# Kernel optimization log

Hardware: AMD Instinct MI355X
Metric: run time of the kernel (lower is better)

## Reference

```python
import jax, jax.numpy as jnp
import numpy as np

V = 50257   # vocab_size
D = 768     # d_model
NL = 4      # n_layers
DI = 1536   # d_inner = expand * d_model
DS = 16     # d_state
DC = 4      # d_conv
B = 2       # batch
L = 512     # seq_len
EPS = 1e-5  # RMSNorm eps
STD = 0.02  # init std


def setup_inputs() -> dict:
    key = jax.random.key(0)
    ks = jax.random.split(key, 8)
    idx = jax.random.randint(ks[0], (B, L), 0, V)
    emb = jax.random.normal(ks[1], (V, D), dtype=jnp.float32) * STD          # tied embedding / lm_head
    W_in = jax.random.normal(ks[2], (NL, 2 * DI, D), dtype=jnp.float32) * STD
    conv_w = jax.random.normal(ks[3], (NL, DI, 1, DC), dtype=jnp.float32) * STD  # depthwise conv [O,I/g,K]
    W_xproj = jax.random.normal(ks[4], (NL, 2 * DS + 1, DI), dtype=jnp.float32) * STD
    W_dt = jax.random.normal(ks[5], (NL, DI, 1), dtype=jnp.float32) * STD    # dt_rank = 1
    b_dt = jnp.zeros((NL, DI), dtype=jnp.float32)
    a_log = jnp.tile(jnp.log(jnp.arange(1, DS + 1, dtype=jnp.float32)), (NL, DI, 1))
    d_param = jnp.ones((NL, DI), dtype=jnp.float32)
    W_out = jax.random.normal(ks[6], (NL, D, DI), dtype=jnp.float32) * STD
    norm_w = jnp.ones((D,), dtype=jnp.float32)
    return dict(idx=idx, emb=emb, W_in=W_in, conv_w=conv_w, W_xproj=W_xproj,
                W_dt=W_dt, b_dt=b_dt, a_log=a_log, d_param=d_param,
                W_out=W_out, norm_w=norm_w)


def _mamba_block(x, W_in, conv_w, W_xproj, W_dt, b_dt, a_log, d_param, W_out):
    # in_proj + split into x, z
    xz = jnp.einsum('bld,ed->ble', x, W_in)            # [B,L,2*DI]
    xs, z = jnp.split(xz, 2, axis=-1)
    # causal depthwise conv1d (torch pads d_conv-1 both sides, keeps first L -> left pad only)
    xc = jnp.transpose(xs, (0, 2, 1))                  # [B,DI,L]
    xc = jax.lax.conv_general_dilated(xc, conv_w, window_strides=(1,),
                                      padding=[(DC - 1, 0)],
                                      feature_group_count=DI,
                                      dimension_numbers=('NCH', 'OIH', 'NCH'))
    xs = jax.nn.silu(jnp.transpose(xc, (0, 2, 1)))     # [B,L,DI]
    # selective SSM
    A = -jnp.exp(a_log)                                # [DI,DS]
    xp = jnp.einsum('bld,ed->ble', xs, W_xproj)        # [B,L,2*DS+1]
    dt_raw = xp[..., 0]                                # [B,L]
    Bp = xp[..., 1:1 + DS]                             # [B,L,DS]
    Cp = xp[..., 1 + DS:]                              # [B,L,DS]
    delta = jax.nn.softplus(dt_raw[..., None] * W_dt[:, 0] + b_dt)  # [B,L,DI]

    def step(h, inp):
        d_i, b_i, c_i, x_i = inp                       # [B,DI],[B,DS],[B,DS],[B,DI]
        a_bar = jnp.exp(d_i[:, :, None] * A)           # [B,DI,DS]
        h = a_bar * h + d_i[:, :, None] * b_i[:, None, :] * x_i[:, :, None]
        y = jnp.einsum('bn,bdn->bd', c_i, h) + d_param * x_i
        return h, y

    h0 = jnp.zeros((x.shape[0], DI, DS), dtype=x.dtype)
    seq = (jnp.moveaxis(delta, 1, 0), jnp.moveaxis(Bp, 1, 0),
           jnp.moveaxis(Cp, 1, 0), jnp.moveaxis(xs, 1, 0))
    _, ys = jax.lax.scan(step, h0, seq)
    y = jnp.moveaxis(ys, 0, 1)                         # [B,L,DI]
    y = y * jax.nn.silu(z)
    return jnp.einsum('ble,de->bld', y, W_out)         # [B,L,D]


def reference(idx, emb, W_in, conv_w, W_xproj, W_dt, b_dt, a_log, d_param, W_out, norm_w):
    x = emb[idx]                                       # [B,L,D]

    def layer(carry, p):
        w_in, c_w, w_xp, w_dt, bdt, alog, dpar, w_out = p
        out = carry + _mamba_block(carry, w_in, c_w, w_xp, w_dt, bdt, alog, dpar, w_out)
        return out, None

    x, _ = jax.lax.scan(layer, x, (W_in, conv_w, W_xproj, W_dt, b_dt, a_log, d_param, W_out))
    rms = jax.lax.rsqrt(jnp.mean(x * x, axis=-1, keepdims=True) + EPS)
    x = x * rms * norm_w
    logits = jnp.einsum('bld,vd->blv', x, emb)         # tied lm_head
    return logits
```

## Files before the change

### kernel.cpp

```cpp
#include <hip/hip_runtime.h>
#include <cstdint>

#define VV     50257
#define VPAD   50432
#define DMODEL 768
#define NLAYER 4
#define DINNER 1536
#define DSTATE 16
#define DCONV  4
#define BATCH  2
#define SEQ    512
#define MROWS  (BATCH*SEQ)
#define XZS    ((long)MROWS * 2 * DINNER)

typedef unsigned short u16;
typedef __attribute__((ext_vector_type(8))) short bf16x8;
typedef __attribute__((ext_vector_type(4))) float f32x4;

__device__ __forceinline__ u16 f2bf(float f) {
  unsigned u = __float_as_uint(f);
  u += 0x7fffu + ((u >> 16) & 1u);
  return (u16)(u >> 16);
}

__device__ __forceinline__ void async16(const void* g, void* l) {
  auto gp = reinterpret_cast<const __attribute__((address_space(1))) unsigned int*>(
      reinterpret_cast<uintptr_t>(g));
  auto lp = reinterpret_cast<__attribute__((address_space(3))) unsigned int*>(
      reinterpret_cast<uintptr_t>(l));
  __builtin_amdgcn_global_load_lds(gp, lp, 16, 0, 0);
}

__global__ void prep_kern(const float* __restrict__ emb, const float* __restrict__ W_in,
                          const float* __restrict__ W_out, const int* __restrict__ idx,
                          u16* __restrict__ embbf, u16* __restrict__ winbf,
                          u16* __restrict__ woutbf, float* __restrict__ xf,
                          u16* __restrict__ xbf) {
  const int E4  = VPAD * DMODEL / 4;
  const int W14 = NLAYER * 2 * DINNER * DMODEL / 4;
  const int W24 = NLAYER * DMODEL * DINNER / 4;
  const int X4  = MROWS * DMODEL / 4;
  const int TOT = E4 + W14 + W24 + X4;
  int i = blockIdx.x * blockDim.x + threadIdx.x;
  const int stride = gridDim.x * blockDim.x;
  for (; i < TOT; i += stride) {
    if (i < E4) {
      ushort4 o;
      if (i < VV * DMODEL / 4) {
        float4 v = *(const float4*)(emb + (long)i * 4);
        o.x = f2bf(v.x); o.y = f2bf(v.y); o.z = f2bf(v.z); o.w = f2bf(v.w);
      } else { o.x = 0; o.y = 0; o.z = 0; o.w = 0; }
      *(ushort4*)(embbf + (long)i * 4) = o;
    } else if (i < E4 + W14) {
      const int j = i - E4;
      float4 v = *(const float4*)(W_in + (long)j * 4);
      ushort4 o; o.x = f2bf(v.x); o.y = f2bf(v.y); o.z = f2bf(v.z); o.w = f2bf(v.w);
      *(ushort4*)(winbf + (long)j * 4) = o;
    } else if (i < E4 + W14 + W24) {
      const int j = i - E4 - W14;
      float4 v = *(const float4*)(W_out + (long)j * 4);
      ushort4 o; o.x = f2bf(v.x); o.y = f2bf(v.y); o.z = f2bf(v.z); o.w = f2bf(v.w);
      *(ushort4*)(woutbf + (long)j * 4) = o;
    } else {
      const int j = i - E4 - W14 - W24;
      const int r = j / (DMODEL / 4);
      const int c = (j % (DMODEL / 4)) * 4;
      const int id = idx[r];
      float4 v = *(const float4*)(emb + (long)id * DMODEL + c);
      *(float4*)(xf + (long)r * DMODEL + c) = v;
      ushort4 o; o.x = f2bf(v.x); o.y = f2bf(v.y); o.z = f2bf(v.z); o.w = f2bf(v.w);
      *(ushort4*)(xbf + (long)r * DMODEL + c) = o;
    }
  }
}

template<bool GUARDN, bool XSWZ>
__global__ __launch_bounds__(256) void gemm3_kern(
    const u16* __restrict__ A, const u16* __restrict__ B,
    float* __restrict__ C, int M, int N, int K, int lda, int ldb)
{
  __shared__ u16 As[3][128 * 32];
  __shared__ u16 Bs[3][128 * 32];
  int bx, by;
  if (XSWZ) {
    const int nt = gridDim.x >> 3;
    const int t = (blockIdx.x & 7) * nt + (blockIdx.x >> 3);
    bx = t & 7; by = t >> 3;
  } else { bx = blockIdx.x; by = blockIdx.y; }
  const int koff = blockIdx.z * K;
  const long coff = (long)blockIdx.z * M * N;

  const int tid  = threadIdx.x;
  const int wave = tid >> 6;
  const int lane = tid & 63;
  const int wr = wave >> 1, wc = wave & 1;
  const int m0 = bx * 128;
  const int n0 = by * 128;

  const int srow = wave * 32 + (lane >> 2);
  const int sblk = ((lane & 3) ^ ((lane >> 3) & 3)) * 8;

  f32x4 acc[4][4];
#pragma unroll
  for (int i = 0; i < 4; ++i)
#pragma unroll
    for (int j = 0; j < 4; ++j) acc[i][j] = (f32x4){0.f, 0.f, 0.f, 0.f};

  const int arow = wr * 64 + (lane & 15);
  const int brow = wc * 64 + (lane & 15);
  const int sa   = (((lane >> 4) ^ ((lane >> 1) & 3)) << 3);

  const int KT = K / 32;
  auto stage = [&](int kt) {
    const int slot = kt % 3;
    const long kcol = (long)koff + kt * 32;
#pragma unroll
    for (int j = 0; j < 2; ++j) {
      async16(A + (long)(m0 + srow + j * 16) * lda + kcol + sblk,
              (char*)(As[slot]) + (wave * 32 + j * 16) * 64);
      async16(B + (long)(n0 + srow + j * 16) * ldb + kcol + sblk,
              (char*)(Bs[slot]) + (wave * 32 + j * 16) * 64);
    }
  };

  stage(0);
  stage(1);
  for (int t = 0; t < KT; ++t) {
    if (t + 2 < KT) {
      stage(t + 2);
      asm volatile("s_waitcnt vmcnt(8)" ::: "memory");
    } else if (t + 2 == KT) {
      asm volatile("s_waitcnt vmcnt(4)" ::: "memory");
    } else {
      asm volatile("s_waitcnt vmcnt(0)" ::: "memory");
    }
    __builtin_amdgcn_s_barrier();
    asm volatile("" ::: "memory");

    const u16* as = As[t % 3];
    const u16* bs = Bs[t % 3];
    bf16x8 af[4], bv[4];
#pragma unroll
    for (int i = 0; i < 4; ++i) af[i] = *(const bf16x8*)(as + (arow + 16 * i) * 32 + sa);
#pragma unroll
    for (int j = 0; j < 4; ++j) bv[j] = *(const bf16x8*)(bs + (brow + 16 * j) * 32 + sa);

    __builtin_amdgcn_s_setprio(1);
#pragma unroll
    for (int i = 0; i < 4; ++i)
#pragma unroll
      for (int j = 0; j < 4; ++j)
        acc[i][j] = __builtin_amdgcn_mfma_f32_16x16x32_bf16(af[i], bv[j], acc[i][j], 0, 0, 0);
    __builtin_amdgcn_s_setprio(0);

    asm volatile("" ::: "memory");
    __builtin_amdgcn_s_barrier();
    asm volatile("" ::: "memory");
  }

  const int rbase = m0 + wr * 64 + ((lane >> 4) << 2);
  const int cbase = n0 + wc * 64 + (lane & 15);
#pragma unroll
  for (int j = 0; j < 4; ++j) {
    const int col = cbase + j * 16;
    if (GUARDN && col >= N) continue;
#pragma unroll
    for (int i = 0; i < 4; ++i) {
#pragma unroll
      for (int r = 0; r < 4; ++r) {
        const int row = rbase + i * 16 + r;
        C[coff + (long)row * N + col] = acc[i][j][r];
      }
    }
  }
}

__global__ __launch_bounds__(512, 2) void gemm8_kern(
    const u16* __restrict__ A, const u16* __restrict__ B,
    float* __restrict__ C, int N, int K, int lda, int ldb)
{
  __shared__ u16 lds[2][2][256 * 64];
  const int tid = threadIdx.x;
  const int wave = tid >> 6;
  const int lane = tid & 63;
  const int wm = wave >> 2, wn = wave & 3;

  const int nwg = gridDim.x;
  const int q = nwg >> 3, r = nwg & 7;
  const int xcd = blockIdx.x & 7;
  const int t = (xcd < r ? xcd * (q + 1) : r * (q + 1) + (xcd - r) * q) + (blockIdx.x >> 3);
  const int m0 = (t & 3) * 256;
  const int n0 = (t >> 2) * 256;

  const int NT = K / 64;

  const int sblk = (((lane & 7) ^ (lane >> 3)) << 3);
  auto stage = [&](int buf, int ab, int half, int kt) {
    const u16* Mat = ab ? B : A;
    const int ld = ab ? ldb : lda;
    const int tb = ab ? n0 : m0;
#pragma unroll
    for (int j = 0; j < 2; ++j) {
      const int rloc = half * 128 + j * 64 + wave * 8;
      async16(Mat + (long)(tb + rloc + (lane >> 3)) * ld + kt * 64 + sblk,
              (char*)&lds[buf][ab][0] + (rloc << 7));
    }
  };

  bf16x8 af[4][2], bl[2][2], bh[2][2];
  const int aq = lane >> 4;
  auto readA = [&](int buf, int half) {
#pragma unroll
    for (int mf = 0; mf < 4; ++mf) {
      const int rr = half * 128 + wm * 64 + mf * 16 + (lane & 15);
#pragma unroll
      for (int ks = 0; ks < 2; ++ks) {
        const int q2 = ks * 4 + aq;
        af[mf][ks] = *(const bf16x8*)(&lds[buf][0][0] + rr * 64 + ((q2 ^ (rr & 7)) << 3));
      }
    }
  };
  auto readB = [&](int buf, int half, bf16x8 (&bf)[2][2]) {
#pragma unroll
    for (int nf = 0; nf < 2; ++nf) {
      const int rr = half * 128 + wn * 32 + nf * 16 + (lane & 15);
#pragma unroll
      for (int ks = 0; ks < 2; ++ks) {
        const int q2 = ks * 4 + aq;
        bf[nf][ks] = *(const bf16x8*)(&lds[buf][1][0] + rr * 64 + ((q2 ^ (rr & 7)) << 3));
      }
    }
  };

  f32x4 acc[8][4];
#pragma unroll
  for (int i = 0; i < 8; ++i)
#pragma unroll
    for (int j = 0; j < 4; ++j) acc[i][j] = (f32x4){0.f, 0.f, 0.f, 0.f};

#define MFMA16(QM, QN, BF)                                                        \
  __builtin_amdgcn_s_setprio(1);                                                  \
  _Pragma("unroll")                                                               \
  for (int mf = 0; mf < 4; ++mf)                                                  \
    _Pragma("unroll")                                                             \
    for (int nf = 0; nf < 2; ++nf)                                                \
      _Pragma("unroll")                                                           \
      for (int ks = 0; ks < 2; ++ks)                                              \
        acc[(QM)*4+mf][(QN)*2+nf] = __builtin_amdgcn_mfma_f32_16x16x32_bf16(      \
            af[mf][ks], BF[nf][ks], acc[(QM)*4+mf][(QN)*2+nf], 0, 0, 0);          \
  __builtin_amdgcn_s_setprio(0);

#define BAR()   asm volatile("" ::: "memory"); __builtin_amdgcn_s_barrier(); asm volatile("" ::: "memory")
#define WAITV(NN) asm volatile("s_waitcnt vmcnt(" #NN ")" ::: "memory"); __builtin_amdgcn_sched_barrier(0)
#define WAITL(NN) asm volatile("s_waitcnt lgkmcnt(" #NN ")" ::: "memory"); __builtin_amdgcn_sched_barrier(0)

  stage(0, 0, 0, 0); stage(0, 1, 0, 0); stage(0, 1, 1, 0); stage(0, 0, 1, 0);
  stage(1, 0, 0, 1); stage(1, 1, 0, 1); stage(1, 1, 1, 1);
  WAITV(6);
  BAR();
  readB(0, 0, bl);

#define TILE(KTE, BUF)                                                            \
  {                                                                               \
    const int kt = (KTE);                                                         \
    if (kt >= NT - 2) { WAITV(0); } else { WAITV(8); }                            \
    BAR();                                                                        \
    readA(BUF, 0);                                                                \
    readB(BUF, 1, bh);                                                            \
    if (kt + 1 < NT) stage(BUF ^ 1, 0, 1, kt + 1);                                \
    WAITL(4);                                                                     \
    MFMA16(0, 0, bl);                                                             \
    BAR();                                                                        \
    if (kt + 2 < NT) stage(BUF, 0, 0, kt + 2);                                    \
    WAITL(0);                                                                     \
    MFMA16(0, 1, bh);                                                             \
    if (kt >= NT - 2) { WAITV(0); } else { WAITV(10); }                           \
    BAR();                                                                        \
    readA(BUF, 1);                                                                \
    if (kt + 2 < NT) stage(BUF, 1, 0, kt + 2);                                    \
    WAITL(0);                                                                     \
    MFMA16(1, 0, bl);                                                             \
    if (kt >= NT - 2) { WAITV(0); } else { WAITV(8); }                            \
    BAR();                                                                        \
    if (kt + 1 < NT) readB(BUF ^ 1, 0, bl);                                       \
    if (kt + 2 < NT) stage(BUF, 1, 1, kt + 2);                                    \
    WAITL(4);                                                                     \
    MFMA16(1, 1, bh);                                                             \
  }

  for (int kt2 = 0; kt2 < NT; kt2 += 2) {
    TILE(kt2, 0);
    TILE(kt2 + 1, 1);
  }

#pragma unroll
  for (int qm = 0; qm < 2; ++qm)
#pragma unroll
    for (int mf = 0; mf < 4; ++mf)
#pragma unroll
      for (int qn = 0; qn < 2; ++qn)
#pragma unroll
        for (int nf = 0; nf < 2; ++nf) {
          const int col = n0 + qn * 128 + wn * 32 + nf * 16 + (lane & 15);
          if (col >= N) continue;
          const int row0 = m0 + qm * 128 + wm * 64 + mf * 16 + ((lane >> 4) << 2);
          const f32x4 v = acc[qm * 4 + mf][qn * 2 + nf];
#pragma unroll
          for (int rr2 = 0; rr2 < 4; ++rr2)
            C[(long)(row0 + rr2) * N + col] = v[rr2];
        }
#undef TILE
#undef MFMA16
#undef BAR
#undef WAITV
#undef WAITL
}

__global__ __launch_bounds__(256) void redout_kern(const float* __restrict__ part,
                                                   float* __restrict__ xf,
                                                   u16* __restrict__ xbf) {
  const int i = blockIdx.x * blockDim.x + threadIdx.x;
  if (i >= MROWS * DMODEL / 4) return;
  const int stride4 = MROWS * DMODEL / 4;
  float4 s = ((const float4*)part)[i];
  float4 p1 = ((const float4*)part)[i + stride4];
  float4 p2 = ((const float4*)part)[i + 2 * stride4];
  float4 p3 = ((const float4*)part)[i + 3 * stride4];
  float4 x = ((const float4*)xf)[i];
  s.x += p1.x + p2.x + p3.x + x.x;
  s.y += p1.y + p2.y + p3.y + x.y;
  s.z += p1.z + p2.z + p3.z + x.z;
  s.w += p1.w + p2.w + p3.w + x.w;
  ((float4*)xf)[i] = s;
  ushort4 o; o.x = f2bf(s.x); o.y = f2bf(s.y); o.z = f2bf(s.z); o.w = f2bf(s.w);
  ((ushort4*)xbf)[i] = o;
}

__global__ __launch_bounds__(256) void convxproj_kern(
    const float* __restrict__ xz, const float* __restrict__ cw,
    const float* __restrict__ Wx, const float* __restrict__ wdt,
    const float* __restrict__ bdt,
    float* __restrict__ xs, float* __restrict__ dlt, float* __restrict__ bc)
{
  __shared__ float sx[DINNER];
  __shared__ float sxp[40];
  const int row = blockIdx.x;
  const int t = row & (SEQ - 1);
  const int tid = threadIdx.x;

  for (int c = tid; c < DINNER; c += 256) {
    const float* w = cw + c * DCONV;
    float a = 0.f;
#pragma unroll
    for (int k = 0; k < DCONV; ++k) {
      const int tt = t - (DCONV - 1) + k;
      if (tt >= 0) {
        const long ix = (long)(row - (DCONV - 1) + k) * (2 * DINNER) + c;
        a += w[k] * (xz[ix] + xz[ix + XZS]);
      }
    }
    const float s = a / (1.f + __expf(-a));
    sx[c] = s;
    xs[(long)row * DINNER + c] = s;
  }
  __syncthreads();

  const int wv = tid >> 6, lane = tid & 63;
  for (int e = wv; e < 2 * DSTATE + 1; e += 4) {
    const float* We = Wx + (long)e * DINNER;
    float p = 0.f;
    for (int d = lane; d < DINNER; d += 64) p += sx[d] * We[d];
#pragma unroll
    for (int off = 32; off; off >>= 1) p += __shfl_xor(p, off, 64);
    if (lane == 0) sxp[e] = p;
  }
  __syncthreads();
  const float dtr = sxp[0];
  for (int d = tid; d < DINNER; d += 256) {
    float v = dtr * wdt[d] + bdt[d];
    float sp = (v > 15.f) ? v : log1pf(__expf(v));
    dlt[(long)row * DINNER + d] = sp;
  }
  if (tid < 2 * DSTATE) bc[(long)row * (2 * DSTATE) + tid] = sxp[1 + tid];
}

__global__ __launch_bounds__(256) void scan_kern(
    const float* __restrict__ dlt, const float* __restrict__ bc,
    const float* __restrict__ xs, const float* __restrict__ xz,
    const float* __restrict__ alog, const float* __restrict__ dpar,
    u16* __restrict__ ybf)
{
  __shared__ float sh_h[32][8][DSTATE];
  __shared__ float sh_s[32][8];
  const int tid = threadIdx.x;
  const int ch = tid & 7, chunk = tid >> 3;
  const int ch_abs = blockIdx.x * 8 + ch;
  const int b = ch_abs / DINNER, d = ch_abs % DINNER;
  float An[DSTATE];
#pragma unroll
  for (int n = 0; n < DSTATE; ++n) An[n] = -__expf(alog[(long)d * DSTATE + n]);
  const int r0 = b * SEQ + chunk * 16;

  float h[DSTATE];
#pragma unroll
  for (int n = 0; n < DSTATE; ++n) h[n] = 0.f;
  float ssum = 0.f;
  for (int s = 0; s < 16; ++s) {
    const int row = r0 + s;
    const float dl = dlt[(long)row * DINNER + d];
    const float xv = xs[(long)row * DINNER + d];
    const float dx = dl * xv;
    const float4* bp = (const float4*)(bc + (long)row * (2 * DSTATE));
    float Bv[DSTATE];
    *(float4*)&Bv[0] = bp[0]; *(float4*)&Bv[4] = bp[1];
    *(float4*)&Bv[8] = bp[2]; *(float4*)&Bv[12] = bp[3];
    ssum += dl;
#pragma unroll
    for (int n = 0; n < DSTATE; ++n) h[n] = __expf(dl * An[n]) * h[n] + dx * Bv[n];
  }
#pragma unroll
  for (int n = 0; n < DSTATE; ++n) sh_h[chunk][ch][n] = h[n];
  sh_s[chunk][ch] = ssum;
  __syncthreads();

  if (tid < 128) {
    const int n2 = tid & 15, ch2 = tid >> 4;
    const int d2 = (blockIdx.x * 8 + ch2) % DINNER;
    const float A2 = -__expf(alog[(long)d2 * DSTATE + n2]);
    float carry = 0.f;
    for (int c = 0; c < 32; ++c) {
      const float hl = sh_h[c][ch2][n2];
      sh_h[c][ch2][n2] = carry;
      carry = __expf(A2 * sh_s[c][ch2]) * carry + hl;
    }
  }
  __syncthreads();

#pragma unroll
  for (int n = 0; n < DSTATE; ++n) h[n] = sh_h[chunk][ch][n];
  const float dp = dpar[d];
  for (int s = 0; s < 16; ++s) {
    const int row = r0 + s;
    const float dl = dlt[(long)row * DINNER + d];
    const float xv = xs[(long)row * DINNER + d];
    const float dx = dl * xv;
    const float4* bp = (const float4*)(bc + (long)row * (2 * DSTATE));
    float Bv[DSTATE], Cv[DSTATE];
    *(float4*)&Bv[0] = bp[0]; *(float4*)&Bv[4] = bp[1];
    *(float4*)&Bv[8] = bp[2]; *(float4*)&Bv[12] = bp[3];
    *(float4*)&Cv[0] = bp[4]; *(float4*)&Cv[4] = bp[5];
    *(float4*)&Cv[8] = bp[6]; *(float4*)&Cv[12] = bp[7];
    float y = 0.f;
#pragma unroll
    for (int n = 0; n < DSTATE; ++n) {
      const float hn = __expf(dl * An[n]) * h[n] + dx * Bv[n];
      h[n] = hn;
      y += Cv[n] * hn;
    }
    y += dp * xv;
    const long zix = (long)row * (2 * DINNER) + DINNER + d;
    const float zz = xz[zix] + xz[zix + XZS];
    const float o = y * (zz / (1.f + __expf(-zz)));
    ybf[(long)row * DINNER + d] = f2bf(o);
  }
}

__global__ __launch_bounds__(256) void rmsfuse_kern(const float* __restrict__ part,
                                                    const float* __restrict__ xf,
                                                    const float* __restrict__ nw,
                                                    u16* __restrict__ xnbf) {
  const int row = blockIdx.x, tid = threadIdx.x;
  const int S = MROWS * DMODEL;
  float v[3];
  float p = 0.f;
#pragma unroll
  for (int k = 0; k < 3; ++k) {
    const int i = row * DMODEL + tid + k * 256;
    float x = xf[i] + part[i] + part[i + S] + part[i + 2 * S] + part[i + 3 * S];
    v[k] = x;
    p += x * x;
  }
#pragma unroll
  for (int off = 32; off; off >>= 1) p += __shfl_xor(p, off, 64);
  __shared__ float red[4];
  __shared__ float s_rms;
  const int wv = tid >> 6, lane = tid & 63;
  if (lane == 0) red[wv] = p;
  __syncthreads();
  if (tid == 0) {
    float tsum = red[0] + red[1] + red[2] + red[3];
    s_rms = rsqrtf(tsum / (float)DMODEL + 1e-5f);
  }
  __syncthreads();
  const float r = s_rms;
#pragma unroll
  for (int k = 0; k < 3; ++k) {
    const int dd = tid + k * 256;
    xnbf[(long)row * DMODEL + dd] = f2bf(v[k] * r * nw[dd]);
  }
}

extern "C" void kernel_launch(void* const* d_in, const int* in_sizes, int n_in,
                              void* d_out, int out_size, void* d_ws, size_t ws_size,
                              hipStream_t stream)
{
  (void)in_sizes; (void)n_in; (void)out_size; (void)ws_size;
  const int*   idx   = (const int*)  d_in[0];
  const float* emb   = (const float*)d_in[1];
  const float* W_in  = (const float*)d_in[2];
  const float* convw = (const float*)d_in[3];
  const float* W_xp  = (const float*)d_in[4];
  const float* W_dt  = (const float*)d_in[5];
  const float* b_dt  = (const float*)d_in[6];
  const float* a_log = (const float*)d_in[7];
  const float* d_par = (const float*)d_in[8];
  const float* W_out = (const float*)d_in[9];
  const float* normw = (const float*)d_in[10];
  float* out = (float*)d_out;

  char* ws = (char*)d_ws;
  size_t off = 0;
  auto alloc = [&](size_t bytes) -> void* {
    void* p = ws + off;
    off += (bytes + 255) & ~(size_t)255;
    return p;
  };
  u16*   embbf  = (u16*)  alloc((size_t)VPAD * DMODEL * 2);
  u16*   winbf  = (u16*)  alloc((size_t)NLAYER * 2 * DINNER * DMODEL * 2);
  u16*   woutbf = (u16*)  alloc((size_t)NLAYER * DMODEL * DINNER * 2);
  float* xf     = (float*)alloc((size_t)MROWS * DMODEL * 4);
  u16*   xbf    = (u16*)  alloc((size_t)MROWS * DMODEL * 2);
  float* xz     = (float*)alloc((size_t)2 * MROWS * 2 * DINNER * 4);
  float* xs     = (float*)alloc((size_t)MROWS * DINNER * 4);
  float* dlt    = (float*)alloc((size_t)MROWS * DINNER * 4);
  float* bc     = (float*)alloc((size_t)MROWS * 2 * DSTATE * 4);
  u16*   ybf    = (u16*)  alloc((size_t)MROWS * DINNER * 2);
  u16*   xnbf   = (u16*)  alloc((size_t)MROWS * DMODEL * 2);
  float* part   = (float*)alloc((size_t)4 * MROWS * DMODEL * 4);

  prep_kern<<<2048, 256, 0, stream>>>(emb, W_in, W_out, idx, embbf, winbf, woutbf, xf, xbf);

  for (int l = 0; l < NLAYER; ++l) {
    gemm3_kern<false, true><<<dim3(8 * (2 * DINNER / 128), 1, 2), 256, 0, stream>>>(
        xbf, winbf + (size_t)l * 2 * DINNER * DMODEL, xz,
        MROWS, 2 * DINNER, DMODEL / 2, DMODEL, DMODEL);
    convxproj_kern<<<MROWS, 256, 0, stream>>>(
        xz, convw + (size_t)l * DINNER * DCONV,
        W_xp + (size_t)l * (2 * DSTATE + 1) * DINNER,
        W_dt + (size_t)l * DINNER, b_dt + (size_t)l * DINNER, xs, dlt, bc);
    scan_kern<<<BATCH * DINNER / 8, 256, 0, stream>>>(
        dlt, bc, xs, xz, a_log + (size_t)l * DINNER * DSTATE, d_par + (size_t)l * DINNER, ybf);
    gemm3_kern<false, true><<<dim3(8 * (DMODEL / 128), 1, 4), 256, 0, stream>>>(
        ybf, woutbf + (size_t)l * DMODEL * DINNER, part,
        MROWS, DMODEL, DINNER / 4, DINNER, DINNER);
    if (l < NLAYER - 1)
      redout_kern<<<MROWS * DMODEL / 4 / 256, 256, 0, stream>>>(part, xf, xbf);
  }
  rmsfuse_kern<<<MROWS, 256, 0, stream>>>(part, xf, normw, xnbf);
  gemm8_kern<<<4 * (VPAD / 256), 512, 0, stream>>>(
      xnbf, embbf, out, VV, DMODEL, DMODEL, DMODEL);
}
```

Measured before the change: 794.5 us.

## Fuse residual add into out-proj via atomics and read fp32 activations in in-proj

Result: slower. 816.2 us (+2.7%).

```diff
diff --git a/kernel.cpp b/kernel.cpp
--- a/kernel.cpp
+++ b/kernel.cpp
@@ -34,8 +34,7 @@
 __global__ void prep_kern(const float* __restrict__ emb, const float* __restrict__ W_in,
                           const float* __restrict__ W_out, const int* __restrict__ idx,
                           u16* __restrict__ embbf, u16* __restrict__ winbf,
-                          u16* __restrict__ woutbf, float* __restrict__ xf,
-                          u16* __restrict__ xbf) {
+                          u16* __restrict__ woutbf, float* __restrict__ xf) {
   const int E4  = VPAD * DMODEL / 4;
   const int W14 = NLAYER * 2 * DINNER * DMODEL / 4;
   const int W24 = NLAYER * DMODEL * DINNER / 4;
@@ -68,27 +67,135 @@
       const int id = idx[r];
       float4 v = *(const float4*)(emb + (long)id * DMODEL + c);
       *(float4*)(xf + (long)r * DMODEL + c) = v;
-      ushort4 o; o.x = f2bf(v.x); o.y = f2bf(v.y); o.z = f2bf(v.z); o.w = f2bf(v.w);
-      *(ushort4*)(xbf + (long)r * DMODEL + c) = o;
-    }
-  }
-}
-
-template<bool GUARDN, bool XSWZ>
+    }
+  }
+}
+
+__global__ __launch_bounds__(256) void gemmf_kern(
+    const float* __restrict__ A, const u16* __restrict__ B,
+    float* __restrict__ C, int M, int N, int K, int lda, int ldb)
+{
+  __shared__ float Af[3][128 * 32];
+  __shared__ u16   Bs[3][128 * 32];
+  const int nt = gridDim.x >> 3;
+  const int t = (blockIdx.x & 7) * nt + (blockIdx.x >> 3);
+  const int bx = t & 7, by = t >> 3;
+  const int koff = blockIdx.z * K;
+  const long coff = (long)blockIdx.z * M * N;
+
+  const int tid  = threadIdx.x;
+  const int wave = tid >> 6;
+  const int lane = tid & 63;
+  const int wr = wave >> 1, wc = wave & 1;
+  const int m0 = bx * 128;
+  const int n0 = by * 128;
+
+  const int sblkA = (((lane & 7) ^ (lane >> 3)) << 2);
+  const int srowB = wave * 32 + (lane >> 2);
+  const int sblkB = ((lane & 3) ^ ((lane >> 3) & 3)) * 8;
+
+  f32x4 acc[4][4];
+#pragma unroll
+  for (int i = 0; i < 4; ++i)
+#pragma unroll
+    for (int j = 0; j < 4; ++j) acc[i][j] = (f32x4){0.f, 0.f, 0.f, 0.f};
+
+  const int arow = wr * 64 + (lane & 15);
+  const int brow = wc * 64 + (lane & 15);
+  const int saB  = (((lane >> 4) ^ ((lane >> 1) & 3)) << 3);
+  const int g2   = (lane >> 4) << 1;
+
+  const int KT = K / 32;
+  auto stage = [&](int kt) {
+    const int slot = kt % 3;
+    const long kcol = (long)koff + kt * 32;
+#pragma unroll
+    for (int j = 0; j < 4; ++j) {
+      const int rloc = wave * 32 + j * 8;
+      async16(A + (long)(m0 + rloc + (lane >> 3)) * lda + kcol + sblkA,
+              (char*)(Af[slot]) + rloc * 128);
+    }
+#pragma unroll
+    for (int j = 0; j < 2; ++j) {
+      async16(B + (long)(n0 + srowB + j * 16) * ldb + kcol + sblkB,
+              (char*)(Bs[slot]) + (wave * 32 + j * 16) * 64);
+    }
+  };
+
+  stage(0);
+  stage(1);
+  for (int t2 = 0; t2 < KT; ++t2) {
+    if (t2 + 2 < KT) {
+      stage(t2 + 2);
+      asm volatile("s_waitcnt vmcnt(12)" ::: "memory");
+    } else if (t2 + 2 == KT) {
+      asm volatile("s_waitcnt vmcnt(6)" ::: "memory");
+    } else {
+      asm volatile("s_waitcnt vmcnt(0)" ::: "memory");
+    }
+    __builtin_amdgcn_s_barrier();
+    asm volatile("" ::: "memory");
+
+    const float* af_l = Af[t2 % 3];
+    const u16*   bs_l = Bs[t2 % 3];
+    bf16x8 av[4], bv[4];
+#pragma unroll
+    for (int i = 0; i < 4; ++i) {
+      const int rr = arow + 16 * i;
+      const float* rp = af_l + rr * 32;
+      const f32x4 lo = *(const f32x4*)(rp + ((g2 ^ (rr & 7)) << 2));
+      const f32x4 hi = *(const f32x4*)(rp + (((g2 + 1) ^ (rr & 7)) << 2));
+      bf16x8 a;
+      a[0] = (short)f2bf(lo[0]); a[1] = (short)f2bf(lo[1]);
+      a[2] = (short)f2bf(lo[2]); a[3] = (short)f2bf(lo[3]);
+      a[4] = (short)f2bf(hi[0]); a[5] = (short)f2bf(hi[1]);
+      a[6] = (short)f2bf(hi[2]); a[7] = (short)f2bf(hi[3]);
+      av[i] = a;
+    }
+#pragma unroll
+    for (int j = 0; j < 4; ++j) bv[j] = *(const bf16x8*)(bs_l + (brow + 16 * j) * 32 + saB);
+
+    __builtin_amdgcn_s_setprio(1);
+#pragma unroll
+    for (int i = 0; i < 4; ++i)
+#pragma unroll
+      for (int j = 0; j < 4; ++j)
+        acc[i][j] = __builtin_amdgcn_mfma_f32_16x16x32_bf16(av[i], bv[j], acc[i][j], 0, 0, 0);
+    __builtin_amdgcn_s_setprio(0);
+
+    asm volatile("" ::: "memory");
+    __builtin_amdgcn_s_barrier();
+    asm volatile("" ::: "memory");
+  }
+
+  const int rbase = m0 + wr * 64 + ((lane >> 4) << 2);
+  const int cbase = n0 + wc * 64 + (lane & 15);
+#pragma unroll
+  for (int j = 0; j < 4; ++j) {
+    const int col = cbase + j * 16;
+#pragma unroll
+    for (int i = 0; i < 4; ++i) {
+#pragma unroll
+      for (int r = 0; r < 4; ++r) {
+        const int row = rbase + i * 16 + r;
+        C[coff + (long)row * N + col] = acc[i][j][r];
+      }
+    }
+  }
+}
+
+template<bool ATOMIC>
 __global__ __launch_bounds__(256) void gemm3_kern(
     const u16* __restrict__ A, const u16* __restrict__ B,
     float* __restrict__ C, int M, int N, int K, int lda, int ldb)
 {
   __shared__ u16 As[3][128 * 32];
   __shared__ u16 Bs[3][128 * 32];
-  int bx, by;
-  if (XSWZ) {
-    const int nt = gridDim.x >> 3;
-    const int t = (blockIdx.x & 7) * nt + (blockIdx.x >> 3);
-    bx = t & 7; by = t >> 3;
-  } else { bx = blockIdx.x; by = blockIdx.y; }
+  const int nt = gridDim.x >> 3;
+  const int t = (blockIdx.x & 7) * nt + (blockIdx.x >> 3);
+  const int bx = t & 7, by = t >> 3;
   const int koff = blockIdx.z * K;
-  const long coff = (long)blockIdx.z * M * N;
+  const long coff = ATOMIC ? 0 : (long)blockIdx.z * M * N;
 
   const int tid  = threadIdx.x;
   const int wave = tid >> 6;
@@ -125,11 +232,11 @@
 
   stage(0);
   stage(1);
-  for (int t = 0; t < KT; ++t) {
-    if (t + 2 < KT) {
-      stage(t + 2);
+  for (int t2 = 0; t2 < KT; ++t2) {
+    if (t2 + 2 < KT) {
+      stage(t2 + 2);
       asm volatile("s_waitcnt vmcnt(8)" ::: "memory");
-    } else if (t + 2 == KT) {
+    } else if (t2 + 2 == KT) {
       asm volatile("s_waitcnt vmcnt(4)" ::: "memory");
     } else {
       asm volatile("s_waitcnt vmcnt(0)" ::: "memory");
@@ -137,8 +244,8 @@
     __builtin_amdgcn_s_barrier();
     asm volatile("" ::: "memory");
 
-    const u16* as = As[t % 3];
-    const u16* bs = Bs[t % 3];
+    const u16* as = As[t2 % 3];
+    const u16* bs = Bs[t2 % 3];
     bf16x8 af[4], bv[4];
 #pragma unroll
     for (int i = 0; i < 4; ++i) af[i] = *(const bf16x8*)(as + (arow + 16 * i) * 32 + sa);
@@ -163,13 +270,18 @@
 #pragma unroll
   for (int j = 0; j < 4; ++j) {
     const int col = cbase + j * 16;
-    if (GUARDN && col >= N) continue;
 #pragma unroll
     for (int i = 0; i < 4; ++i) {
 #pragma unroll
       for (int r = 0; r < 4; ++r) {
         const int row = rbase + i * 16 + r;
-        C[coff + (long)row * N + col] = acc[i][j][r];
+        const long off = coff + (long)row * N + col;
+        if (ATOMIC) {
+          __hip_atomic_fetch_add(&C[off], acc[i][j][r], __ATOMIC_RELAXED,
+                                 __HIP_MEMORY_SCOPE_AGENT);
+        } else {
+          C[off] = acc[i][j][r];
+        }
       }
     }
   }
@@ -316,26 +428,6 @@
 #undef WAITL
 }
 
-__global__ __launch_bounds__(256) void redout_kern(const float* __restrict__ part,
-                                                   float* __restrict__ xf,
-                                                   u16* __restrict__ xbf) {
-  const int i = blockIdx.x * blockDim.x + threadIdx.x;
-  if (i >= MROWS * DMODEL / 4) return;
-  const int stride4 = MROWS * DMODEL / 4;
-  float4 s = ((const float4*)part)[i];
-  float4 p1 = ((const float4*)part)[i + stride4];
-  float4 p2 = ((const float4*)part)[i + 2 * stride4];
-  float4 p3 = ((const float4*)part)[i + 3 * stride4];
-  float4 x = ((const float4*)xf)[i];
-  s.x += p1.x + p2.x + p3.x + x.x;
-  s.y += p1.y + p2.y + p3.y + x.y;
-  s.z += p1.z + p2.z + p3.z + x.z;
-  s.w += p1.w + p2.w + p3.w + x.w;
-  ((float4*)xf)[i] = s;
-  ushort4 o; o.x = f2bf(s.x); o.y = f2bf(s.y); o.z = f2bf(s.z); o.w = f2bf(s.w);
-  ((ushort4*)xbf)[i] = o;
-}
-
 __global__ __launch_bounds__(256) void convxproj_kern(
     const float* __restrict__ xz, const float* __restrict__ cw,
     const float* __restrict__ Wx, const float* __restrict__ wdt,
@@ -465,20 +557,17 @@
   }
 }
 
-__global__ __launch_bounds__(256) void rmsfuse_kern(const float* __restrict__ part,
-                                                    const float* __restrict__ xf,
-                                                    const float* __restrict__ nw,
-                                                    u16* __restrict__ xnbf) {
+__global__ __launch_bounds__(256) void rms_kern(const float* __restrict__ xf,
+                                                const float* __restrict__ nw,
+                                                u16* __restrict__ xnbf) {
   const int row = blockIdx.x, tid = threadIdx.x;
-  const int S = MROWS * DMODEL;
   float v[3];
   float p = 0.f;
 #pragma unroll
   for (int k = 0; k < 3; ++k) {
     const int i = row * DMODEL + tid + k * 256;
-    float x = xf[i] + part[i] + part[i + S] + part[i + 2 * S] + part[i + 3 * S];
-    v[k] = x;
-    p += x * x;
+    v[k] = xf[i];
+    p += v[k] * v[k];
   }
 #pragma unroll
   for (int off = 32; off; off >>= 1) p += __shfl_xor(p, off, 64);
@@ -529,20 +618,18 @@
   u16*   winbf  = (u16*)  alloc((size_t)NLAYER * 2 * DINNER * DMODEL * 2);
   u16*   woutbf = (u16*)  alloc((size_t)NLAYER * DMODEL * DINNER * 2);
   float* xf     = (float*)alloc((size_t)MROWS * DMODEL * 4);
-  u16*   xbf    = (u16*)  alloc((size_t)MROWS * DMODEL * 2);
   float* xz     = (float*)alloc((size_t)2 * MROWS * 2 * DINNER * 4);
   float* xs     = (float*)alloc((size_t)MROWS * DINNER * 4);
   float* dlt    = (float*)alloc((size_t)MROWS * DINNER * 4);
   float* bc     = (float*)alloc((size_t)MROWS * 2 * DSTATE * 4);
   u16*   ybf    = (u16*)  alloc((size_t)MROWS * DINNER * 2);
   u16*   xnbf   = (u16*)  alloc((size_t)MROWS * DMODEL * 2);
-  float* part   = (float*)alloc((size_t)4 * MROWS * DMODEL * 4);
-
-  prep_kern<<<2048, 256, 0, stream>>>(emb, W_in, W_out, idx, embbf, winbf, woutbf, xf, xbf);
+
+  prep_kern<<<2048, 256, 0, stream>>>(emb, W_in, W_out, idx, embbf, winbf, woutbf, xf);
 
   for (int l = 0; l < NLAYER; ++l) {
-    gemm3_kern<false, true><<<dim3(8 * (2 * DINNER / 128), 1, 2), 256, 0, stream>>>(
-        xbf, winbf + (size_t)l * 2 * DINNER * DMODEL, xz,
+    gemmf_kern<<<dim3(8 * (2 * DINNER / 128), 1, 2), 256, 0, stream>>>(
+        xf, winbf + (size_t)l * 2 * DINNER * DMODEL, xz,
         MROWS, 2 * DINNER, DMODEL / 2, DMODEL, DMODEL);
     convxproj_kern<<<MROWS, 256, 0, stream>>>(
         xz, convw + (size_t)l * DINNER * DCONV,
@@ -550,13 +637,11 @@
         W_dt + (size_t)l * DINNER, b_dt + (size_t)l * DINNER, xs, dlt, bc);
     scan_kern<<<BATCH * DINNER / 8, 256, 0, stream>>>(
         dlt, bc, xs, xz, a_log + (size_t)l * DINNER * DSTATE, d_par + (size_t)l * DINNER, ybf);
-    gemm3_kern<false, true><<<dim3(8 * (DMODEL / 128), 1, 4), 256, 0, stream>>>(
-        ybf, woutbf + (size_t)l * DMODEL * DINNER, part,
+    gemm3_kern<true><<<dim3(8 * (DMODEL / 128), 1, 4), 256, 0, stream>>>(
+        ybf, woutbf + (size_t)l * DMODEL * DINNER, xf,
         MROWS, DMODEL, DINNER / 4, DINNER, DINNER);
-    if (l < NLAYER - 1)
-      redout_kern<<<MROWS * DMODEL / 4 / 256, 256, 0, stream>>>(part, xf, xbf);
-  }
-  rmsfuse_kern<<<MROWS, 256, 0, stream>>>(part, xf, normw, xnbf);
+  }
+  rms_kern<<<MROWS, 256, 0, stream>>>(xf, normw, xnbf);
   gemm8_kern<<<4 * (VPAD / 256), 512, 0, stream>>>(
       xnbf, embbf, out, VV, DMODEL, DMODEL, DMODEL);
 }
```

## Replace lm_head GEMM with 256x128 tile, 2-stage pipeline, higher occupancy

Applied to the files above, without the earlier changes.

New measurement: 813.7 us. +2.4%, slower.

```diff
diff --git a/kernel.cpp b/kernel.cpp
--- a/kernel.cpp
+++ b/kernel.cpp
@@ -125,11 +125,11 @@
 
   stage(0);
   stage(1);
-  for (int t = 0; t < KT; ++t) {
-    if (t + 2 < KT) {
-      stage(t + 2);
+  for (int t2 = 0; t2 < KT; ++t2) {
+    if (t2 + 2 < KT) {
+      stage(t2 + 2);
       asm volatile("s_waitcnt vmcnt(8)" ::: "memory");
-    } else if (t + 2 == KT) {
+    } else if (t2 + 2 == KT) {
       asm volatile("s_waitcnt vmcnt(4)" ::: "memory");
     } else {
       asm volatile("s_waitcnt vmcnt(0)" ::: "memory");
@@ -137,8 +137,8 @@
     __builtin_amdgcn_s_barrier();
     asm volatile("" ::: "memory");
 
-    const u16* as = As[t % 3];
-    const u16* bs = Bs[t % 3];
+    const u16* as = As[t2 % 3];
+    const u16* bs = Bs[t2 % 3];
     bf16x8 af[4], bv[4];
 #pragma unroll
     for (int i = 0; i < 4; ++i) af[i] = *(const bf16x8*)(as + (arow + 16 * i) * 32 + sa);
@@ -175,145 +175,106 @@
   }
 }
 
-__global__ __launch_bounds__(512, 2) void gemm8_kern(
+__global__ __launch_bounds__(512, 4) void gemm9_kern(
     const u16* __restrict__ A, const u16* __restrict__ B,
     float* __restrict__ C, int N, int K, int lda, int ldb)
 {
-  __shared__ u16 lds[2][2][256 * 64];
+  __shared__ u16 As[2][256 * 32];
+  __shared__ u16 Bs[2][128 * 32];
   const int tid = threadIdx.x;
   const int wave = tid >> 6;
   const int lane = tid & 63;
-  const int wm = wave >> 2, wn = wave & 3;
-
-  const int nwg = gridDim.x;
-  const int q = nwg >> 3, r = nwg & 7;
-  const int xcd = blockIdx.x & 7;
-  const int t = (xcd < r ? xcd * (q + 1) : r * (q + 1) + (xcd - r) * q) + (blockIdx.x >> 3);
+  const int wm = wave >> 1, wn = wave & 1;
+
+  const int nt = gridDim.x >> 3;
+  const int t = (blockIdx.x & 7) * nt + (blockIdx.x >> 3);
   const int m0 = (t & 3) * 256;
-  const int n0 = (t >> 2) * 256;
-
-  const int NT = K / 64;
-
-  const int sblk = (((lane & 7) ^ (lane >> 3)) << 3);
-  auto stage = [&](int buf, int ab, int half, int kt) {
-    const u16* Mat = ab ? B : A;
-    const int ld = ab ? ldb : lda;
-    const int tb = ab ? n0 : m0;
+  const int n0 = (t >> 2) * 128;
+
+  const int NT = K / 32;
+
+  auto stage = [&](int buf, int kt) {
+    const long kc = (long)kt * 32;
 #pragma unroll
     for (int j = 0; j < 2; ++j) {
-      const int rloc = half * 128 + j * 64 + wave * 8;
-      async16(Mat + (long)(tb + rloc + (lane >> 3)) * ld + kt * 64 + sblk,
-              (char*)&lds[buf][ab][0] + (rloc << 7));
+      const int rl = wave * 32 + j * 16 + (lane >> 2);
+      const int sb = (((lane & 3) ^ ((rl >> 1) & 3)) << 3);
+      async16(A + (long)(m0 + rl) * lda + kc + sb,
+              (char*)(As[buf]) + (wave * 32 + j * 16) * 64);
+    }
+    {
+      const int rl = wave * 16 + (lane >> 2);
+      const int sb = (((lane & 3) ^ ((rl >> 1) & 3)) << 3);
+      async16(B + (long)(n0 + rl) * ldb + kc + sb,
+              (char*)(Bs[buf]) + (wave * 16) * 64);
     }
   };
 
-  bf16x8 af[4][2], bl[2][2], bh[2][2];
+  f32x4 acc[4][4];
+#pragma unroll
+  for (int i = 0; i < 4; ++i)
+#pragma unroll
+    for (int j = 0; j < 4; ++j) acc[i][j] = (f32x4){0.f, 0.f, 0.f, 0.f};
+
   const int aq = lane >> 4;
-  auto readA = [&](int buf, int half) {
+  const int lrow = lane & 15;
+
+  stage(0, 0);
+  stage(1, 1);
+  for (int kt = 0; kt < NT; ++kt) {
+    const int buf = kt & 1;
+    if (kt + 1 < NT) {
+      asm volatile("s_waitcnt vmcnt(3)" ::: "memory");
+    } else {
+      asm volatile("s_waitcnt vmcnt(0)" ::: "memory");
+    }
+    __builtin_amdgcn_sched_barrier(0);
+    __builtin_amdgcn_s_barrier();
+    asm volatile("" ::: "memory");
+
+    bf16x8 af[4], bb[4];
 #pragma unroll
     for (int mf = 0; mf < 4; ++mf) {
-      const int rr = half * 128 + wm * 64 + mf * 16 + (lane & 15);
-#pragma unroll
-      for (int ks = 0; ks < 2; ++ks) {
-        const int q2 = ks * 4 + aq;
-        af[mf][ks] = *(const bf16x8*)(&lds[buf][0][0] + rr * 64 + ((q2 ^ (rr & 7)) << 3));
-      }
-    }
-  };
-  auto readB = [&](int buf, int half, bf16x8 (&bf)[2][2]) {
-#pragma unroll
-    for (int nf = 0; nf < 2; ++nf) {
-      const int rr = half * 128 + wn * 32 + nf * 16 + (lane & 15);
-#pragma unroll
-      for (int ks = 0; ks < 2; ++ks) {
-        const int q2 = ks * 4 + aq;
-        bf[nf][ks] = *(const bf16x8*)(&lds[buf][1][0] + rr * 64 + ((q2 ^ (rr & 7)) << 3));
-      }
-    }
-  };
-
-  f32x4 acc[8][4];
-#pragma unroll
-  for (int i = 0; i < 8; ++i)
-#pragma unroll
-    for (int j = 0; j < 4; ++j) acc[i][j] = (f32x4){0.f, 0.f, 0.f, 0.f};
-
-#define MFMA16(QM, QN, BF)                                                        \
-  __builtin_amdgcn_s_setprio(1);                                                  \
-  _Pragma("unroll")                                                               \
-  for (int mf = 0; mf < 4; ++mf)                                                  \
-    _Pragma("unroll")                                                             \
-    for (int nf = 0; nf < 2; ++nf)                                                \
-      _Pragma("unroll")                                                           \
-      for (int ks = 0; ks < 2; ++ks)                                              \
-        acc[(QM)*4+mf][(QN)*2+nf] = __builtin_amdgcn_mfma_f32_16x16x32_bf16(      \
-            af[mf][ks], BF[nf][ks], acc[(QM)*4+mf][(QN)*2+nf], 0, 0, 0);          \
-  __builtin_amdgcn_s_setprio(0);
-
-#define BAR()   asm volatile("" ::: "memory"); __builtin_amdgcn_s_barrier(); asm volatile("" ::: "memory")
-#define WAITV(NN) asm volatile("s_waitcnt vmcnt(" #NN ")" ::: "memory"); __builtin_amdgcn_sched_barrier(0)
-#define WAITL(NN) asm volatile("s_waitcnt lgkmcnt(" #NN ")" ::: "memory"); __builtin_amdgcn_sched_barrier(0)
-
-  stage(0, 0, 0, 0); stage(0, 1, 0, 0); stage(0, 1, 1, 0); stage(0, 0, 1, 0);
-  stage(1, 0, 0, 1); stage(1, 1, 0, 1); stage(1, 1, 1, 1);
-  WAITV(6);
-  BAR();
-  readB(0, 0, bl);
-
-#define TILE(KTE, BUF)                                                            \
-  {                                                                               \
-    const int kt = (KTE);                                                         \
-    if (kt >= NT - 2) { WAITV(0); } else { WAITV(8); }                            \
-    BAR();                                                                        \
-    readA(BUF, 0);                                                                \
-    readB(BUF, 1, bh);                                                            \
-    if (kt + 1 < NT) stage(BUF ^ 1, 0, 1, kt + 1);                                \
-    WAITL(4);                                                                     \
-    MFMA16(0, 0, bl);                                                             \
-    BAR();                                                                        \
-    if (kt + 2 < NT) stage(BUF, 0, 0, kt + 2);                                    \
-    WAITL(0);                                                                     \
-    MFMA16(0, 1, bh);                                                             \
-    if (kt >= NT - 2) { WAITV(0); } else { WAITV(10); }                           \
-    BAR();                                                                        \
-    readA(BUF, 1);                                                                \
-    if (kt + 2 < NT) stage(BUF, 1, 0, kt + 2);                                    \
-    WAITL(0);                                                                     \
-    MFMA16(1, 0, bl);                                                             \
-    if (kt >= NT - 2) { WAITV(0); } else { WAITV(8); }                            \
-    BAR();                                                                        \
-    if (kt + 1 < NT) readB(BUF ^ 1, 0, bl);                                       \
-    if (kt + 2 < NT) stage(BUF, 1, 1, kt + 2);                                    \
-    WAITL(4);                                                                     \
-    MFMA16(1, 1, bh);                                                             \
-  }
-
-  for (int kt2 = 0; kt2 < NT; kt2 += 2) {
-    TILE(kt2, 0);
-    TILE(kt2 + 1, 1);
-  }
-
-#pragma unroll
-  for (int qm = 0; qm < 2; ++qm)
+      const int rr = wm * 64 + mf * 16 + lrow;
+      af[mf] = *(const bf16x8*)(As[buf] + rr * 32 + ((aq ^ ((rr >> 1) & 3)) << 3));
+    }
+#pragma unroll
+    for (int nf = 0; nf < 4; ++nf) {
+      const int rr = wn * 64 + nf * 16 + lrow;
+      bb[nf] = *(const bf16x8*)(Bs[buf] + rr * 32 + ((aq ^ ((rr >> 1) & 3)) << 3));
+    }
+    asm volatile("s_waitcnt lgkmcnt(0)" ::: "memory");
+    __builtin_amdgcn_sched_barrier(0);
+
+    __builtin_amdgcn_s_setprio(1);
 #pragma unroll
     for (int mf = 0; mf < 4; ++mf)
 #pragma unroll
-      for (int qn = 0; qn < 2; ++qn)
-#pragma unroll
-        for (int nf = 0; nf < 2; ++nf) {
-          const int col = n0 + qn * 128 + wn * 32 + nf * 16 + (lane & 15);
-          if (col >= N) continue;
-          const int row0 = m0 + qm * 128 + wm * 64 + mf * 16 + ((lane >> 4) << 2);
-          const f32x4 v = acc[qm * 4 + mf][qn * 2 + nf];
-#pragma unroll
-          for (int rr2 = 0; rr2 < 4; ++rr2)
-            C[(long)(row0 + rr2) * N + col] = v[rr2];
-        }
-#undef TILE
-#undef MFMA16
-#undef BAR
-#undef WAITV
-#undef WAITL
+      for (int nf = 0; nf < 4; ++nf)
+        acc[mf][nf] = __builtin_amdgcn_mfma_f32_16x16x32_bf16(af[mf], bb[nf], acc[mf][nf], 0, 0, 0);
+    __builtin_amdgcn_s_setprio(0);
+
+    asm volatile("" ::: "memory");
+    __builtin_amdgcn_s_barrier();
+    asm volatile("" ::: "memory");
+    if (kt + 2 < NT) stage(buf, kt + 2);
+  }
+
+  const int rbase = m0 + wm * 64 + ((lane >> 4) << 2);
+  const int cbase = n0 + wn * 64 + (lane & 15);
+#pragma unroll
+  for (int nf = 0; nf < 4; ++nf) {
+    const int col = cbase + nf * 16;
+    if (col >= N) continue;
+#pragma unroll
+    for (int mf = 0; mf < 4; ++mf) {
+      const int row0 = rbase + mf * 16;
+      const f32x4 v = acc[mf][nf];
+#pragma unroll
+      for (int r = 0; r < 4; ++r)
+        C[(long)(row0 + r) * N + col] = v[r];
+    }
+  }
 }
 
 __global__ __launch_bounds__(256) void redout_kern(const float* __restrict__ part,
@@ -557,6 +518,6 @@
       redout_kern<<<MROWS * DMODEL / 4 / 256, 256, 0, stream>>>(part, xf, xbf);
   }
   rmsfuse_kern<<<MROWS, 256, 0, stream>>>(part, xf, normw, xnbf);
-  gemm8_kern<<<4 * (VPAD / 256), 512, 0, stream>>>(
+  gemm9_kern<<<4 * (VPAD / 128), 512, 0, stream>>>(
       xnbf, embbf, out, VV, DMODEL, DMODEL, DMODEL);
 }
```

## Make LM-head GEMM persistent and raise out-projection split-K to eight

Applied to the files above, without the earlier changes.

Measured after the change: 816.6 us. 1.03x slower.

```diff
diff --git a/kernel.cpp b/kernel.cpp
--- a/kernel.cpp
+++ b/kernel.cpp
@@ -12,6 +12,7 @@
 #define SEQ    512
 #define MROWS  (BATCH*SEQ)
 #define XZS    ((long)MROWS * 2 * DINNER)
+#define OPS    ((long)MROWS * DMODEL)
 
 typedef unsigned short u16;
 typedef __attribute__((ext_vector_type(8))) short bf16x8;
@@ -125,11 +126,11 @@
 
   stage(0);
   stage(1);
-  for (int t = 0; t < KT; ++t) {
-    if (t + 2 < KT) {
-      stage(t + 2);
+  for (int t2 = 0; t2 < KT; ++t2) {
+    if (t2 + 2 < KT) {
+      stage(t2 + 2);
       asm volatile("s_waitcnt vmcnt(8)" ::: "memory");
-    } else if (t + 2 == KT) {
+    } else if (t2 + 2 == KT) {
       asm volatile("s_waitcnt vmcnt(4)" ::: "memory");
     } else {
       asm volatile("s_waitcnt vmcnt(0)" ::: "memory");
@@ -137,8 +138,8 @@
     __builtin_amdgcn_s_barrier();
     asm volatile("" ::: "memory");
 
-    const u16* as = As[t % 3];
-    const u16* bs = Bs[t % 3];
+    const u16* as = As[t2 % 3];
+    const u16* bs = Bs[t2 % 3];
     bf16x8 af[4], bv[4];
 #pragma unroll
     for (int i = 0; i < 4; ++i) af[i] = *(const bf16x8*)(as + (arow + 16 * i) * 32 + sa);
@@ -184,21 +185,17 @@
   const int wave = tid >> 6;
   const int lane = tid & 63;
   const int wm = wave >> 2, wn = wave & 3;
-
-  const int nwg = gridDim.x;
-  const int q = nwg >> 3, r = nwg & 7;
-  const int xcd = blockIdx.x & 7;
-  const int t = (xcd < r ? xcd * (q + 1) : r * (q + 1) + (xcd - r) * q) + (blockIdx.x >> 3);
-  const int m0 = (t & 3) * 256;
-  const int n0 = (t >> 2) * 256;
-
   const int NT = K / 64;
 
+  const int r = blockIdx.x;
+  const int cnt  = 3 + (r < 20 ? 1 : 0);
+  const int base = 3 * r + (r < 20 ? r : 20);
+
   const int sblk = (((lane & 7) ^ (lane >> 3)) << 3);
-  auto stage = [&](int buf, int ab, int half, int kt) {
+  auto stage = [&](int buf, int ab, int half, int kt, int sm0, int sn0) {
     const u16* Mat = ab ? B : A;
     const int ld = ab ? ldb : lda;
-    const int tb = ab ? n0 : m0;
+    const int tb = ab ? sn0 : sm0;
 #pragma unroll
     for (int j = 0; j < 2; ++j) {
       const int rloc = half * 128 + j * 64 + wave * 8;
@@ -233,10 +230,6 @@
   };
 
   f32x4 acc[8][4];
-#pragma unroll
-  for (int i = 0; i < 8; ++i)
-#pragma unroll
-    for (int j = 0; j < 4; ++j) acc[i][j] = (f32x4){0.f, 0.f, 0.f, 0.f};
 
 #define MFMA16(QM, QN, BF)                                                        \
   __builtin_amdgcn_s_setprio(1);                                                  \
@@ -254,62 +247,88 @@
 #define WAITV(NN) asm volatile("s_waitcnt vmcnt(" #NN ")" ::: "memory"); __builtin_amdgcn_sched_barrier(0)
 #define WAITL(NN) asm volatile("s_waitcnt lgkmcnt(" #NN ")" ::: "memory"); __builtin_amdgcn_sched_barrier(0)
 
-  stage(0, 0, 0, 0); stage(0, 1, 0, 0); stage(0, 1, 1, 0); stage(0, 0, 1, 0);
-  stage(1, 0, 0, 1); stage(1, 1, 0, 1); stage(1, 1, 1, 1);
-  WAITV(6);
-  BAR();
-  readB(0, 0, bl);
-
-#define TILE(KTE, BUF)                                                            \
+#define PROLOGUE(M0, N0)                                                          \
+  stage(0, 0, 0, 0, M0, N0); stage(0, 1, 0, 0, M0, N0);                           \
+  stage(0, 1, 1, 0, M0, N0); stage(0, 0, 1, 0, M0, N0);                           \
+  stage(1, 0, 0, 1, M0, N0); stage(1, 1, 0, 1, M0, N0);                           \
+  stage(1, 1, 1, 1, M0, N0);
+
+#define TILE(KTE, BUF, TM0, TN0)                                                  \
   {                                                                               \
     const int kt = (KTE);                                                         \
     if (kt >= NT - 2) { WAITV(0); } else { WAITV(8); }                            \
     BAR();                                                                        \
     readA(BUF, 0);                                                                \
     readB(BUF, 1, bh);                                                            \
-    if (kt + 1 < NT) stage(BUF ^ 1, 0, 1, kt + 1);                                \
+    if (kt + 1 < NT) stage(BUF ^ 1, 0, 1, kt + 1, TM0, TN0);                      \
     WAITL(4);                                                                     \
     MFMA16(0, 0, bl);                                                             \
     BAR();                                                                        \
-    if (kt + 2 < NT) stage(BUF, 0, 0, kt + 2);                                    \
+    if (kt + 2 < NT) stage(BUF, 0, 0, kt + 2, TM0, TN0);                          \
     WAITL(0);                                                                     \
     MFMA16(0, 1, bh);                                                             \
     if (kt >= NT - 2) { WAITV(0); } else { WAITV(10); }                           \
     BAR();                                                                        \
     readA(BUF, 1);                                                                \
-    if (kt + 2 < NT) stage(BUF, 1, 0, kt + 2);                                    \
+    if (kt + 2 < NT) stage(BUF, 1, 0, kt + 2, TM0, TN0);                          \
     WAITL(0);                                                                     \
     MFMA16(1, 0, bl);                                                             \
     if (kt >= NT - 2) { WAITV(0); } else { WAITV(8); }                            \
     BAR();                                                                        \
     if (kt + 1 < NT) readB(BUF ^ 1, 0, bl);                                       \
-    if (kt + 2 < NT) stage(BUF, 1, 1, kt + 2);                                    \
+    if (kt + 2 < NT) stage(BUF, 1, 1, kt + 2, TM0, TN0);                          \
     WAITL(4);                                                                     \
     MFMA16(1, 1, bh);                                                             \
   }
 
-  for (int kt2 = 0; kt2 < NT; kt2 += 2) {
-    TILE(kt2, 0);
-    TILE(kt2 + 1, 1);
-  }
-
-#pragma unroll
-  for (int qm = 0; qm < 2; ++qm)
-#pragma unroll
-    for (int mf = 0; mf < 4; ++mf)
-#pragma unroll
-      for (int qn = 0; qn < 2; ++qn)
-#pragma unroll
-        for (int nf = 0; nf < 2; ++nf) {
-          const int col = n0 + qn * 128 + wn * 32 + nf * 16 + (lane & 15);
-          if (col >= N) continue;
-          const int row0 = m0 + qm * 128 + wm * 64 + mf * 16 + ((lane >> 4) << 2);
-          const f32x4 v = acc[qm * 4 + mf][qn * 2 + nf];
-#pragma unroll
-          for (int rr2 = 0; rr2 < 4; ++rr2)
-            C[(long)(row0 + rr2) * N + col] = v[rr2];
-        }
+  {
+    const int u0 = base;
+    PROLOGUE((u0 & 3) * 256, (u0 >> 2) * 256);
+  }
+
+#pragma unroll 1
+  for (int i = 0; i < cnt; ++i) {
+    const int u = base + i;
+    const int cm0 = (u & 3) * 256;
+    const int cn0 = (u >> 2) * 256;
+
+#pragma unroll
+    for (int a2 = 0; a2 < 8; ++a2)
+#pragma unroll
+      for (int b2 = 0; b2 < 4; ++b2) acc[a2][b2] = (f32x4){0.f, 0.f, 0.f, 0.f};
+
+    WAITV(6);
+    BAR();
+    readB(0, 0, bl);
+
+    for (int kt2 = 0; kt2 < NT; kt2 += 2) {
+      TILE(kt2, 0, cm0, cn0);
+      TILE(kt2 + 1, 1, cm0, cn0);
+    }
+    if (i + 1 < cnt) {
+      const int un = u + 1;
+      PROLOGUE((un & 3) * 256, (un >> 2) * 256);
+    }
+
+#pragma unroll
+    for (int qm = 0; qm < 2; ++qm)
+#pragma unroll
+      for (int mf = 0; mf < 4; ++mf)
+#pragma unroll
+        for (int qn = 0; qn < 2; ++qn)
+#pragma unroll
+          for (int nf = 0; nf < 2; ++nf) {
+            const int col = cn0 + qn * 128 + wn * 32 + nf * 16 + (lane & 15);
+            if (col >= N) continue;
+            const int row0 = cm0 + qm * 128 + wm * 64 + mf * 16 + ((lane >> 4) << 2);
+            const f32x4 v = acc[qm * 4 + mf][qn * 2 + nf];
+#pragma unroll
+            for (int rr2 = 0; rr2 < 4; ++rr2)
+              C[(long)(row0 + rr2) * N + col] = v[rr2];
+          }
+  }
 #undef TILE
+#undef PROLOGUE
 #undef MFMA16
 #undef BAR
 #undef WAITV
@@ -322,15 +341,12 @@
   const int i = blockIdx.x * blockDim.x + threadIdx.x;
   if (i >= MROWS * DMODEL / 4) return;
   const int stride4 = MROWS * DMODEL / 4;
-  float4 s = ((const float4*)part)[i];
-  float4 p1 = ((const float4*)part)[i + stride4];
-  float4 p2 = ((const float4*)part)[i + 2 * stride4];
-  float4 p3 = ((const float4*)part)[i + 3 * stride4];
-  float4 x = ((const float4*)xf)[i];
-  s.x += p1.x + p2.x + p3.x + x.x;
-  s.y += p1.y + p2.y + p3.y + x.y;
-  s.z += p1.z + p2.z + p3.z + x.z;
-  s.w += p1.w + p2.w + p3.w + x.w;
+  float4 s = ((const float4*)xf)[i];
+#pragma unroll
+  for (int k = 0; k < 8; ++k) {
+    float4 p = ((const float4*)part)[i + k * stride4];
+    s.x += p.x; s.y += p.y; s.z += p.z; s.w += p.w;
+  }
   ((float4*)xf)[i] = s;
   ushort4 o; o.x = f2bf(s.x); o.y = f2bf(s.y); o.z = f2bf(s.z); o.w = f2bf(s.w);
   ((ushort4*)xbf)[i] = o;
@@ -470,13 +486,14 @@
                                                     const float* __restrict__ nw,
                                                     u16* __restrict__ xnbf) {
   const int row = blockIdx.x, tid = threadIdx.x;
-  const int S = MROWS * DMODEL;
   float v[3];
   float p = 0.f;
 #pragma unroll
   for (int k = 0; k < 3; ++k) {
     const int i = row * DMODEL + tid + k * 256;
-    float x = xf[i] + part[i] + part[i + S] + part[i + 2 * S] + part[i + 3 * S];
+    float x = xf[i];
+#pragma unroll
+    for (int q = 0; q < 8; ++q) x += part[i + q * OPS];
     v[k] = x;
     p += x * x;
   }
@@ -536,9 +553,8 @@
   float* bc     = (float*)alloc((size_t)MROWS * 2 * DSTATE * 4);
   u16*   ybf    = (u16*)  alloc((size_t)MROWS * DINNER * 2);
   u16*   xnbf   = (u16*)  alloc((size_t)MROWS * DMODEL * 2);
-  float* part   = (float*)alloc((size_t)4 * MROWS * DMODEL * 4);
-
-  prep_kern<<<2048, 256, 0, stream>>>(emb, W_in, W_out, idx, embbf, winbf, woutbf, xf, xbf);
+
+  prep_kern<<<3072, 256, 0, stream>>>(emb, W_in, W_out, idx, embbf, winbf, woutbf, xf, xbf);
 
   for (int l = 0; l < NLAYER; ++l) {
     gemm3_kern<false, true><<<dim3(8 * (2 * DINNER / 128), 1, 2), 256, 0, stream>>>(
@@ -550,13 +566,13 @@
         W_dt + (size_t)l * DINNER, b_dt + (size_t)l * DINNER, xs, dlt, bc);
     scan_kern<<<BATCH * DINNER / 8, 256, 0, stream>>>(
         dlt, bc, xs, xz, a_log + (size_t)l * DINNER * DSTATE, d_par + (size_t)l * DINNER, ybf);
-    gemm3_kern<false, true><<<dim3(8 * (DMODEL / 128), 1, 4), 256, 0, stream>>>(
-        ybf, woutbf + (size_t)l * DMODEL * DINNER, part,
-        MROWS, DMODEL, DINNER / 4, DINNER, DINNER);
+    gemm3_kern<false, true><<<dim3(8 * (DMODEL / 128), 1, 8), 256, 0, stream>>>(
+        ybf, woutbf + (size_t)l * DMODEL * DINNER, xz,
+        MROWS, DMODEL, DINNER / 8, DINNER, DINNER);
     if (l < NLAYER - 1)
-      redout_kern<<<MROWS * DMODEL / 4 / 256, 256, 0, stream>>>(part, xf, xbf);
-  }
-  rmsfuse_kern<<<MROWS, 256, 0, stream>>>(part, xf, normw, xnbf);
-  gemm8_kern<<<4 * (VPAD / 256), 512, 0, stream>>>(
+      redout_kern<<<MROWS * DMODEL / 4 / 256, 256, 0, stream>>>(xz, xf, xbf);
+  }
+  rmsfuse_kern<<<MROWS, 256, 0, stream>>>(xz, xf, normw, xnbf);
+  gemm8_kern<<<256, 512, 0, stream>>>(
       xnbf, embbf, out, VV, DMODEL, DMODEL, DMODEL);
 }
```
